# Kernel optimization log

Measured on AMD Instinct MI355X. Metric: run time of the kernel, lower is better.

## Reference

```python
import jax, jax.numpy as jnp
import numpy as np

DIM, HEADS, DHEAD = 256, 8, 64
HID = HEADS * DHEAD


def _elu1(x):
    # F.elu(x) + 1 == exp(x) for x<0, x+1 for x>=0
    return jnp.where(x > 0, x + 1.0, jnp.exp(x))


def setup_inputs() -> dict:
    key = jax.random.key(0)
    ks = jax.random.split(key, 6)
    B, H, W = 8, 64, 64
    x = jax.random.normal(ks[0], (B, DIM, H, W), dtype=jnp.float32)
    contact_map = jax.random.uniform(ks[1], (B, 1, H, W), dtype=jnp.float32)
    s_qkv = 1.0 / np.sqrt(DIM)
    Wqkv = jax.random.normal(ks[2], (3 * HID, DIM), dtype=jnp.float32) * s_qkv
    s_out = 1.0 / np.sqrt(HID)
    Wout = jax.random.normal(ks[3], (DIM, HID), dtype=jnp.float32) * s_out
    bout = jax.random.normal(ks[4], (DIM,), dtype=jnp.float32) * 0.01
    contact_scale = jnp.float32(0.1)
    return {"x": x, "contact_map": contact_map, "Wqkv": Wqkv,
            "Wout": Wout, "bout": bout, "contact_scale": contact_scale}


def reference(x, contact_map, Wqkv, Wout, bout, contact_scale):
    b, c, h, w = x.shape
    n = h * w
    xf = x.reshape(b, c, n)                                  # b c n
    qkv = jnp.einsum('oc,bcn->bon', Wqkv, xf)                # b (3*H*D) n
    qkv = qkv.reshape(b, 3, HEADS, DHEAD, n)                 # qkv-major channel order
    q = _elu1(qkv[:, 0])                                     # b h d n
    k = _elu1(qkv[:, 1])
    v = qkv[:, 2]
    cm = contact_map.reshape(b, 1, 1, n)                     # b 1 1 n
    k = k * (1.0 + contact_scale * cm)
    kv = jnp.einsum('bhdn,bhen->bhde', k, v)                 # b h d e
    ksum = k.sum(axis=-1)                                    # b h d
    z = 1.0 / (jnp.einsum('bhdn,bhd->bhn', q, ksum) + 1e-6)  # b h n
    out = jnp.einsum('bhde,bhdn->bhne', kv, q) * z[..., None]  # b h n e
    out = out.transpose(0, 1, 3, 2).reshape(b, HID, n)       # b (h d) n
    y = jnp.einsum('oc,bcn->bon', Wout, out) + bout[None, :, None]
    return y.reshape(b, -1, h, w)
```

## Files before the change

### kernel.cpp

```cpp
#include <hip/hip_runtime.h>
#include <stdint.h>


#define NPIX 4096
#define HIDC 512
#define DIMC 256
#define BATCH 8

typedef __attribute__((ext_vector_type(8))) short bf16x8;
typedef __attribute__((ext_vector_type(4))) float f32x4;
typedef __attribute__((ext_vector_type(16))) float f32x16;

__device__ __forceinline__ float bf2f(unsigned short h) {
    unsigned int u = ((unsigned int)h) << 16; float f;
    __builtin_memcpy(&f, &u, 4); return f;
}
__device__ __forceinline__ unsigned short f2bf(float f) {
    unsigned int u; __builtin_memcpy(&u, &f, 4);
    u += 0x7fffu + ((u >> 16) & 1u);
    return (unsigned short)(u >> 16);
}
__device__ __forceinline__ float elu1(float x) {
    return x > 0.f ? x + 1.f : __expf(x);
}
__device__ __forceinline__ void gl16(const unsigned short* g, unsigned short* l) {
    __builtin_amdgcn_global_load_lds(
        (__attribute__((address_space(1))) const void*)g,
        (__attribute__((address_space(3))) void*)l, 16, 0, 0);
}

__global__ __launch_bounds__(256) void k_convW(
    const float* __restrict__ Wqkv, const float* __restrict__ Wout,
    unsigned short* __restrict__ Wb, unsigned short* __restrict__ Wob)
{
    int i4 = (blockIdx.x * 256 + threadIdx.x) * 4;
    const int NW1 = 1536 * 256;
    float4 v; unsigned short* dst;
    if (i4 < NW1) { v = *(const float4*)&Wqkv[i4]; dst = Wb + i4; }
    else { int j = i4 - NW1; v = *(const float4*)&Wout[j]; dst = Wob + j; }
    ushort4 o; o.x = f2bf(v.x); o.y = f2bf(v.y); o.z = f2bf(v.z); o.w = f2bf(v.w);
    *(ushort4*)dst = o;
}

__global__ __launch_bounds__(256) void k_tx(
    const float* __restrict__ x, unsigned short* __restrict__ xT)
{
    __shared__ float tile[32][33];
    const int n0 = blockIdx.x * 32, c0 = blockIdx.y * 32, b = blockIdx.z;
    const int t = threadIdx.x;
    const int r = t >> 3, c4 = (t & 7) * 4;
    float4 v = *(const float4*)&x[((size_t)b * DIMC + c0 + r) * NPIX + n0 + c4];
    tile[r][c4 + 0] = v.x; tile[r][c4 + 1] = v.y;
    tile[r][c4 + 2] = v.z; tile[r][c4 + 3] = v.w;
    __syncthreads();
    ushort4 o;
    unsigned short* op = (unsigned short*)&o;
#pragma unroll
    for (int i = 0; i < 4; i++) op[i] = f2bf(tile[c4 + i][r]);
    *(ushort4*)&xT[((size_t)b * NPIX + n0 + r) * DIMC + c0 + c4] = o;
}

__global__ __launch_bounds__(256) void k_qkv(
    const unsigned short* __restrict__ xT,
    const unsigned short* __restrict__ Wb,
    const float* __restrict__ cmp,
    const float* __restrict__ csp,
    unsigned short* __restrict__ qT,
    unsigned short* __restrict__ kb,
    unsigned short* __restrict__ vb)
{
    const int b  = blockIdx.z;
    const int m0 = blockIdx.x * 128;
    const int n0 = blockIdx.y * 128;
    const int t = threadIdx.x;
    const int wave = t >> 6, lane = t & 63;
    const int wm = wave >> 1, wn = wave & 1;
    const int l31 = lane & 31, lhi = lane >> 5;
    const int sect = n0 >> 9;

    __shared__ unsigned short As[128 * 64];
    __shared__ unsigned short Bs[128 * 64];

    const unsigned short* Ag = xT + ((size_t)b * NPIX + m0) * DIMC;
    const unsigned short* Bg = Wb + (size_t)n0 * DIMC;

    const unsigned short* mArr = (sect == 0) ? As : Bs;
    const unsigned short* nArr = (sect == 0) ? Bs : As;

    f32x16 acc[2][2];
#pragma unroll
    for (int i = 0; i < 2; i++)
#pragma unroll
        for (int j = 0; j < 2; j++)
#pragma unroll
            for (int r = 0; r < 16; r++) acc[i][j][r] = 0.f;

    const int r8  = lane >> 3;
    const int jg8 = (((lane & 7) ^ r8) & 7) * 8;
    const int xsw = (l31 & 7);

    for (int k0 = 0; k0 < DIMC; k0 += 64) {
#pragma unroll
        for (int i = 0; i < 4; i++) {
            const int rowg = wave * 32 + i * 8;
            gl16(&Ag[(size_t)(rowg + r8) * DIMC + k0 + jg8], &As[rowg * 64]);
            gl16(&Bg[(size_t)(rowg + r8) * DIMC + k0 + jg8], &Bs[rowg * 64]);
        }
        __syncthreads();
#pragma unroll
        for (int ks = 0; ks < 4; ks++) {
            const int coff = ((ks * 2 + lhi) ^ xsw) * 8;
            bf16x8 af[2], bfg[2];
#pragma unroll
            for (int fm = 0; fm < 2; fm++)
                af[fm] = *(const bf16x8*)&mArr[(wm * 64 + fm * 32 + l31) * 64 + coff];
#pragma unroll
            for (int fn = 0; fn < 2; fn++)
                bfg[fn] = *(const bf16x8*)&nArr[(wn * 64 + fn * 32 + l31) * 64 + coff];
#pragma unroll
            for (int fm = 0; fm < 2; fm++)
#pragma unroll
                for (int fn = 0; fn < 2; fn++)
                    acc[fm][fn] = __builtin_amdgcn_mfma_f32_32x32x16_bf16(
                        af[fm], bfg[fn], acc[fm][fn], 0, 0, 0);
        }
        __syncthreads();
    }

    const float cs = *csp;
    if (sect == 0) {
#pragma unroll
        for (int fm = 0; fm < 2; fm++) {
            const int pbase = m0 + wm * 64 + fm * 32;
#pragma unroll
            for (int fn = 0; fn < 2; fn++) {
                const int o = n0 + wn * 64 + fn * 32 + l31;
#pragma unroll
                for (int r = 0; r < 16; r++) {
                    int prow = pbase + (r & 3) + 8 * (r >> 2) + 4 * lhi;
                    qT[((size_t)b * NPIX + prow) * HIDC + o] = f2bf(elu1(acc[fm][fn][r]));
                }
            }
        }
    } else {
        unsigned short* dstb = (sect == 1) ? kb : vb;
#pragma unroll
        for (int fm = 0; fm < 2; fm++) {
            const int obase = (n0 & 511) + wm * 64 + fm * 32;
#pragma unroll
            for (int fn = 0; fn < 2; fn++) {
                const int pixel = m0 + wn * 64 + fn * 32 + l31;
                float g = 1.f;
                if (sect == 1) g = 1.f + cs * cmp[(size_t)b * NPIX + pixel];
#pragma unroll
                for (int r = 0; r < 16; r++) {
                    int orow = obase + (r & 3) + 8 * (r >> 2) + 4 * lhi;
                    float val = acc[fm][fn][r];
                    if (sect == 1) val = elu1(val) * g;
                    dstb[((size_t)b * HIDC + orow) * NPIX + pixel] = f2bf(val);
                }
            }
        }
    }
}

#define LS2 40
__global__ __launch_bounds__(256) void k_kv(
    const unsigned short* __restrict__ kb, const unsigned short* __restrict__ vb,
    float* __restrict__ kv, float* __restrict__ ksum)
{
    const int bh = blockIdx.y, nc = blockIdx.x;
    const int t = threadIdx.x, wave = t >> 6, lane = t & 63;
    const int lrow = lane & 15, quad = lane >> 4;

    __shared__ unsigned short ks[64 * LS2];
    __shared__ unsigned short vs[64 * LS2];

    const size_t base = (size_t)bh * 64 * NPIX;
    f32x4 acc[4];
#pragma unroll
    for (int i = 0; i < 4; i++) acc[i] = (f32x4){0.f, 0.f, 0.f, 0.f};
    float ksacc = 0.f;

    const int row = t >> 2, c8 = (t & 3) * 8;

    for (int step = 0; step < 16; step++) {
        const int ncol = nc * 512 + step * 32;
        uint4 kq = *(const uint4*)&kb[base + (size_t)row * NPIX + ncol + c8];
        *(uint4*)&ks[row * LS2 + c8] = kq;
        *(uint4*)&vs[row * LS2 + c8] = *(const uint4*)&vb[base + (size_t)row * NPIX + ncol + c8];
        const unsigned short* kp = (const unsigned short*)&kq;
#pragma unroll
        for (int j = 0; j < 8; j++) ksacc += bf2f(kp[j]);
        __syncthreads();
        bf16x8 bfv = *(const bf16x8*)&vs[(wave * 16 + lrow) * LS2 + quad * 8];
#pragma unroll
        for (int mt = 0; mt < 4; mt++) {
            bf16x8 af = *(const bf16x8*)&ks[(mt * 16 + lrow) * LS2 + quad * 8];
            acc[mt] = __builtin_amdgcn_mfma_f32_16x16x32_bf16(af, bfv, acc[mt], 0, 0, 0);
        }
        __syncthreads();
    }

    float* kvb = kv + (size_t)bh * 4096;
#pragma unroll
    for (int mt = 0; mt < 4; mt++)
#pragma unroll
        for (int r = 0; r < 4; r++)
            atomicAdd(&kvb[(mt * 16 + quad * 4 + r) * 64 + wave * 16 + lrow], acc[mt][r]);
    atomicAdd(&ksum[bh * 64 + row], ksacc);
}

#define LS3 72
__global__ __launch_bounds__(256) void k_out(
    const unsigned short* __restrict__ qT,
    const float* __restrict__ kv, const float* __restrict__ ksum,
    unsigned short* __restrict__ outT)
{
    const int bh = blockIdx.y, p0 = blockIdx.x * 128;
    const int b = bh >> 3, h = bh & 7;
    const int t = threadIdx.x, wave = t >> 6, lane = t & 63;
    const int l31 = lane & 31, lhi = lane >> 5;

    __shared__ unsigned short Aq[128 * LS3];
    __shared__ unsigned short Bv[96 * LS3];

    const unsigned short* qg = qT + ((size_t)b * NPIX + p0) * HIDC + h * 64;
#pragma unroll
    for (int i = 0; i < 4; i++) {
        int idx = t + i * 256;
        int row = idx >> 3, c8 = (idx & 7) * 8;
        *(uint4*)&Aq[row * LS3 + c8] = *(const uint4*)&qg[(size_t)row * HIDC + c8];
    }
    const float* kvg = kv + (size_t)bh * 4096;
#pragma unroll
    for (int i = 0; i < 16; i++) {
        int idx = t + i * 256;
        int d = idx >> 6, e = idx & 63;
        Bv[e * LS3 + d] = f2bf(kvg[idx]);
    }
    if (t < 64) {
        float ksv = ksum[bh * 64 + t];
        unsigned short hi = f2bf(ksv);
        Bv[64 * LS3 + t] = hi;
        Bv[65 * LS3 + t] = f2bf(ksv - bf2f(hi));
    }
    for (int i = t; i < 30 * 64; i += 256)
        Bv[(66 + (i >> 6)) * LS3 + (i & 63)] = 0;
    __syncthreads();

    f32x16 acc[3];
#pragma unroll
    for (int j = 0; j < 3; j++)
#pragma unroll
        for (int r = 0; r < 16; r++) acc[j][r] = 0.f;

#pragma unroll
    for (int ksub = 0; ksub < 4; ksub++) {
        const int koff = ksub * 16 + lhi * 8;
        bf16x8 af = *(const bf16x8*)&Aq[(wave * 32 + l31) * LS3 + koff];
#pragma unroll
        for (int nf = 0; nf < 3; nf++) {
            bf16x8 bfg = *(const bf16x8*)&Bv[(nf * 32 + l31) * LS3 + koff];
            acc[nf] = __builtin_amdgcn_mfma_f32_32x32x16_bf16(af, bfg, acc[nf], 0, 0, 0);
        }
    }

    unsigned short* og = outT + ((size_t)b * NPIX + p0 + wave * 32) * HIDC + h * 64;
#pragma unroll
    for (int r = 0; r < 16; r++) {
        float hi = __shfl(acc[2][r], lane & 32);
        float lo = __shfl(acc[2][r], (lane & 32) | 1);
        float z = 1.f / (hi + lo + 1e-6f);
        int prow = (r & 3) + 8 * (r >> 2) + 4 * lhi;
#pragma unroll
        for (int nf = 0; nf < 2; nf++)
            og[(size_t)prow * HIDC + nf * 32 + l31] = f2bf(acc[nf][r] * z);
    }
}

__global__ __launch_bounds__(256) void k_y(
    const unsigned short* __restrict__ outT,
    const unsigned short* __restrict__ Wob,
    const float* __restrict__ bout,
    float* __restrict__ y)
{
    const int b  = blockIdx.z;
    const int m0 = blockIdx.x * 128;
    const int n0 = blockIdx.y * 128;
    const int t = threadIdx.x;
    const int wave = t >> 6, lane = t & 63;
    const int wm = wave >> 1, wn = wave & 1;
    const int lrow = lane & 15, quad = lane >> 4;

    __shared__ unsigned short As[128 * 64];
    __shared__ unsigned short Bs[128 * 64];

    const unsigned short* Ag = outT + ((size_t)b * NPIX + m0) * HIDC;
    const unsigned short* Bg = Wob + (size_t)n0 * HIDC;

    f32x4 acc[4][4];
#pragma unroll
    for (int i = 0; i < 4; i++)
#pragma unroll
        for (int j = 0; j < 4; j++) acc[i][j] = (f32x4){0.f, 0.f, 0.f, 0.f};

    const int r8  = lane >> 3;
    const int jg8 = (((lane & 7) ^ r8) & 7) * 8;
    const int xswA = (lrow & 7);

    for (int k0 = 0; k0 < HIDC; k0 += 64) {
#pragma unroll
        for (int i = 0; i < 4; i++) {
            const int rowg = wave * 32 + i * 8;
            gl16(&Ag[(size_t)(rowg + r8) * HIDC + k0 + jg8], &As[rowg * 64]);
            gl16(&Bg[(size_t)(rowg + r8) * HIDC + k0 + jg8], &Bs[rowg * 64]);
        }
        __syncthreads();
#pragma unroll
        for (int ksb = 0; ksb < 2; ksb++) {
            bf16x8 af[4], bfr[4];
#pragma unroll
            for (int mt = 0; mt < 4; mt++) {
                const int row = wm * 64 + mt * 16 + lrow;
                af[mt] = *(const bf16x8*)&As[row * 64 + (((ksb * 4 + quad) ^ xswA)) * 8];
            }
#pragma unroll
            for (int nt = 0; nt < 4; nt++) {
                const int row = wn * 64 + nt * 16 + lrow;
                bfr[nt] = *(const bf16x8*)&Bs[row * 64 + (((ksb * 4 + quad) ^ xswA)) * 8];
            }
#pragma unroll
            for (int mt = 0; mt < 4; mt++)
#pragma unroll
                for (int nt = 0; nt < 4; nt++)
                    acc[mt][nt] = __builtin_amdgcn_mfma_f32_16x16x32_bf16(
                        af[mt], bfr[nt], acc[mt][nt], 0, 0, 0);
        }
        __syncthreads();
    }

#pragma unroll
    for (int mt = 0; mt < 4; mt++) {
        const int pixel0 = m0 + wm * 64 + mt * 16 + quad * 4;
#pragma unroll
        for (int nt = 0; nt < 4; nt++) {
            const int o = n0 + wn * 64 + nt * 16 + lrow;
            const float bias = bout[o];
            f32x4 a = acc[mt][nt];
            float4 st; st.x = a[0] + bias; st.y = a[1] + bias;
            st.z = a[2] + bias; st.w = a[3] + bias;
            *(float4*)&y[((size_t)b * DIMC + o) * NPIX + pixel0] = st;
        }
    }
}

extern "C" void kernel_launch(void* const* d_in, const int* in_sizes, int n_in,
                              void* d_out, int out_size, void* d_ws, size_t ws_size,
                              hipStream_t stream) {
    (void)in_sizes; (void)n_in; (void)out_size; (void)ws_size;
    const float* x    = (const float*)d_in[0];
    const float* cm   = (const float*)d_in[1];
    const float* Wqkv = (const float*)d_in[2];
    const float* Wout = (const float*)d_in[3];
    const float* bout = (const float*)d_in[4];
    const float* csp  = (const float*)d_in[5];
    float* y = (float*)d_out;

    const size_t qn = (size_t)BATCH * HIDC * NPIX;
    char* ws = (char*)d_ws;
    unsigned short* qT   = (unsigned short*)ws;                 ws += qn * 2;
    unsigned short* kb   = (unsigned short*)ws;                 ws += qn * 2;
    unsigned short* vb   = (unsigned short*)ws;                 ws += qn * 2;
    unsigned short* outT = (unsigned short*)ws;                 ws += qn * 2;
    unsigned short* xT   = outT;
    float* kvp   = (float*)ws;                                  ws += (size_t)64 * 64 * 64 * 4;
    float* ksump = (float*)ws;                                  ws += (size_t)64 * 64 * 4;
    unsigned short* Wb  = (unsigned short*)ws;                  ws += (size_t)1536 * 256 * 2;
    unsigned short* Wob = (unsigned short*)ws;

    hipMemsetAsync(kvp, 0, ((size_t)64 * 64 * 64 + 64 * 64) * sizeof(float), stream);
    k_convW<<<512, 256, 0, stream>>>(Wqkv, Wout, Wb, Wob);
    k_tx  <<<dim3(128, 8, 8), 256, 0, stream>>>(x, xT);
    k_qkv <<<dim3(32, 12, 8), 256, 0, stream>>>(xT, Wb, cm, csp, qT, kb, vb);
    k_kv  <<<dim3(8, 64),     256, 0, stream>>>(kb, vb, kvp, ksump);
    k_out <<<dim3(32, 64),    256, 0, stream>>>(qT, kvp, ksump, outT);
    k_y   <<<dim3(32, 2, 8),  256, 0, stream>>>(outT, Wob, bout, y);
}
```

Baseline: 207.9 us.

## Fuse QKV projection with KV and ksum reduction in a single kernel

Replaces the separate QKV GEMM and kv-reduction kernels with one kernel per (pixel tile, batch) that computes q to global memory, but keeps k and v head tiles in shared memory and immediately reduces them into kv and ksum via MFMA and atomics. This removes writing and re-reading the full k and v tensors through global memory and one kernel launch. In exchange the grid is much smaller with one block per CU, work is serialised across heads with many barriers, and more atomic adds hit kv.

```diff
diff --git a/kernel.cpp b/kernel.cpp
--- a/kernel.cpp
+++ b/kernel.cpp
@@ -60,155 +60,154 @@
     *(ushort4*)&xT[((size_t)b * NPIX + n0 + r) * DIMC + c0 + c4] = o;
 }
 
-__global__ __launch_bounds__(256) void k_qkv(
+
+#define COMPUTE_TILE(SWAP, A0, A1)                                             \
+    {                                                                          \
+        const unsigned short* Wl = &Ws[cur][0];                                \
+        _Pragma("unroll")                                                      \
+        for (int ks = 0; ks < 16; ks++) {                                      \
+            bf16x8 wf = *(const bf16x8*)&Wl[(wn * 32 + l31) * DIMC +           \
+                                (((ks * 2 + lhi) ^ (l31 & 7)) * 8)];           \
+            if (SWAP) {                                                        \
+                A0 = __builtin_amdgcn_mfma_f32_32x32x16_bf16(wf, af[0][ks], A0, 0, 0, 0); \
+                A1 = __builtin_amdgcn_mfma_f32_32x32x16_bf16(wf, af[1][ks], A1, 0, 0, 0); \
+            } else {                                                           \
+                A0 = __builtin_amdgcn_mfma_f32_32x32x16_bf16(af[0][ks], wf, A0, 0, 0, 0); \
+                A1 = __builtin_amdgcn_mfma_f32_32x32x16_bf16(af[1][ks], wf, A1, 0, 0, 0); \
+            }                                                                  \
+        }                                                                      \
+    }
+
+__global__ __launch_bounds__(256, 1) void k_fused(
     const unsigned short* __restrict__ xT,
     const unsigned short* __restrict__ Wb,
     const float* __restrict__ cmp,
     const float* __restrict__ csp,
     unsigned short* __restrict__ qT,
-    unsigned short* __restrict__ kb,
-    unsigned short* __restrict__ vb)
-{
-    const int b  = blockIdx.z;
+    float* __restrict__ kvp,
+    float* __restrict__ ksump)
+{
+    const int b  = blockIdx.y;
     const int m0 = blockIdx.x * 128;
-    const int n0 = blockIdx.y * 128;
-    const int t = threadIdx.x;
+    const int t  = threadIdx.x;
     const int wave = t >> 6, lane = t & 63;
     const int wm = wave >> 1, wn = wave & 1;
     const int l31 = lane & 31, lhi = lane >> 5;
-    const int sect = n0 >> 9;
-
-    __shared__ unsigned short As[128 * 64];
-    __shared__ unsigned short Bs[128 * 64];
-
-    const unsigned short* Ag = xT + ((size_t)b * NPIX + m0) * DIMC;
-    const unsigned short* Bg = Wb + (size_t)n0 * DIMC;
-
-    const unsigned short* mArr = (sect == 0) ? As : Bs;
-    const unsigned short* nArr = (sect == 0) ? Bs : As;
-
-    f32x16 acc[2][2];
-#pragma unroll
-    for (int i = 0; i < 2; i++)
-#pragma unroll
-        for (int j = 0; j < 2; j++)
-#pragma unroll
-            for (int r = 0; r < 16; r++) acc[i][j][r] = 0.f;
-
-    const int r8  = lane >> 3;
-    const int jg8 = (((lane & 7) ^ r8) & 7) * 8;
-    const int xsw = (l31 & 7);
-
-    for (int k0 = 0; k0 < DIMC; k0 += 64) {
-#pragma unroll
-        for (int i = 0; i < 4; i++) {
-            const int rowg = wave * 32 + i * 8;
-            gl16(&Ag[(size_t)(rowg + r8) * DIMC + k0 + jg8], &As[rowg * 64]);
-            gl16(&Bg[(size_t)(rowg + r8) * DIMC + k0 + jg8], &Bs[rowg * 64]);
-        }
-        __syncthreads();
-#pragma unroll
-        for (int ks = 0; ks < 4; ks++) {
-            const int coff = ((ks * 2 + lhi) ^ xsw) * 8;
-            bf16x8 af[2], bfg[2];
-#pragma unroll
-            for (int fm = 0; fm < 2; fm++)
-                af[fm] = *(const bf16x8*)&mArr[(wm * 64 + fm * 32 + l31) * 64 + coff];
-#pragma unroll
-            for (int fn = 0; fn < 2; fn++)
-                bfg[fn] = *(const bf16x8*)&nArr[(wn * 64 + fn * 32 + l31) * 64 + coff];
-#pragma unroll
-            for (int fm = 0; fm < 2; fm++)
-#pragma unroll
-                for (int fn = 0; fn < 2; fn++)
-                    acc[fm][fn] = __builtin_amdgcn_mfma_f32_32x32x16_bf16(
-                        af[fm], bfg[fn], acc[fm][fn], 0, 0, 0);
-        }
-        __syncthreads();
-    }
+
+    __shared__ unsigned short Ws[2][64 * DIMC];
+    __shared__ unsigned short kS[64 * 128];
+    __shared__ unsigned short vS[64 * 128];
 
     const float cs = *csp;
-    if (sect == 0) {
-#pragma unroll
-        for (int fm = 0; fm < 2; fm++) {
-            const int pbase = m0 + wm * 64 + fm * 32;
-#pragma unroll
-            for (int fn = 0; fn < 2; fn++) {
-                const int o = n0 + wn * 64 + fn * 32 + l31;
-#pragma unroll
-                for (int r = 0; r < 16; r++) {
-                    int prow = pbase + (r & 3) + 8 * (r >> 2) + 4 * lhi;
-                    qT[((size_t)b * NPIX + prow) * HIDC + o] = f2bf(elu1(acc[fm][fn][r]));
-                }
+
+    auto stageW = [&](int wr, int buf) {
+#pragma unroll
+        for (int i = 0; i < 8; i++) {
+            const int rowl = wave * 16 + i * 2 + (lane >> 5);
+            const int ck = (lane & 31) ^ (rowl & 7);
+            gl16(&Wb[(size_t)(wr + rowl) * DIMC + ck * 8],
+                 &Ws[buf][(wave * 16 + i * 2) * DIMC]);
+        }
+    };
+
+    stageW(0, 0);
+
+    bf16x8 af[2][16];
+    {
+        const unsigned short* Ab = xT + ((size_t)b * NPIX + m0 + wm * 64) * DIMC;
+#pragma unroll
+        for (int pt = 0; pt < 2; pt++)
+#pragma unroll
+            for (int ks = 0; ks < 16; ks++)
+                af[pt][ks] = *(const bf16x8*)&Ab[(size_t)(pt * 32 + l31) * DIMC
+                                                 + ks * 16 + lhi * 8];
+    }
+
+    const float gv0 = 1.f + cs * cmp[(size_t)b * NPIX + m0 + wm * 64 + l31];
+    const float gv1 = 1.f + cs * cmp[(size_t)b * NPIX + m0 + wm * 64 + 32 + l31];
+
+    __syncthreads();
+    int cur = 0;
+
+    for (int nt = 0; nt < 8; nt++) {
+        stageW(nt < 7 ? (nt + 1) * 64 : 512, cur ^ 1);
+        f32x16 acc0, acc1;
+#pragma unroll
+        for (int r = 0; r < 16; r++) { acc0[r] = 0.f; acc1[r] = 0.f; }
+        COMPUTE_TILE(0, acc0, acc1)
+        const int chq = nt * 64 + wn * 32 + l31;
+        unsigned short* qg = qT + ((size_t)b * NPIX + m0 + wm * 64) * HIDC + chq;
+#pragma unroll
+        for (int r = 0; r < 16; r++) {
+            const int rp = (r & 3) + 8 * (r >> 2) + 4 * lhi;
+            qg[(size_t)rp * HIDC]        = f2bf(elu1(acc0[r]));
+            qg[(size_t)(32 + rp) * HIDC] = f2bf(elu1(acc1[r]));
+        }
+        __syncthreads();
+        cur ^= 1;
+    }
+
+    for (int h = 0; h < 8; h++) {
+        stageW(1024 + h * 64, cur ^ 1);
+        f32x16 acc0, acc1;
+#pragma unroll
+        for (int r = 0; r < 16; r++) { acc0[r] = 0.f; acc1[r] = 0.f; }
+        COMPUTE_TILE(1, acc0, acc1)
+#pragma unroll
+        for (int r = 0; r < 16; r++) {
+            const int ch = wn * 32 + (r & 3) + 8 * (r >> 2) + 4 * lhi;
+            const int sw = (ch & 7) << 3;
+            const int p0 = wm * 64 + l31;
+            kS[ch * 128 + (p0 ^ sw)]        = f2bf(elu1(acc0[r]) * gv0);
+            kS[ch * 128 + ((p0 + 32) ^ sw)] = f2bf(elu1(acc1[r]) * gv1);
+        }
+        __syncthreads();
+        {
+            const int ch = t & 63, cb = (t >> 6) * 4;
+            float s = 0.f;
+#pragma unroll
+            for (int j = 0; j < 4; j++) {
+                const bf16x8 kr = *(const bf16x8*)&kS[ch * 128 + (((cb + j) ^ (ch & 7)) * 8)];
+#pragma unroll
+                for (int u = 0; u < 8; u++) s += bf2f(((const unsigned short*)&kr)[u]);
             }
-        }
-    } else {
-        unsigned short* dstb = (sect == 1) ? kb : vb;
-#pragma unroll
-        for (int fm = 0; fm < 2; fm++) {
-            const int obase = (n0 & 511) + wm * 64 + fm * 32;
-#pragma unroll
-            for (int fn = 0; fn < 2; fn++) {
-                const int pixel = m0 + wn * 64 + fn * 32 + l31;
-                float g = 1.f;
-                if (sect == 1) g = 1.f + cs * cmp[(size_t)b * NPIX + pixel];
-#pragma unroll
-                for (int r = 0; r < 16; r++) {
-                    int orow = obase + (r & 3) + 8 * (r >> 2) + 4 * lhi;
-                    float val = acc[fm][fn][r];
-                    if (sect == 1) val = elu1(val) * g;
-                    dstb[((size_t)b * HIDC + orow) * NPIX + pixel] = f2bf(val);
-                }
-            }
-        }
-    }
-}
-
-#define LS2 40
-__global__ __launch_bounds__(256) void k_kv(
-    const unsigned short* __restrict__ kb, const unsigned short* __restrict__ vb,
-    float* __restrict__ kv, float* __restrict__ ksum)
-{
-    const int bh = blockIdx.y, nc = blockIdx.x;
-    const int t = threadIdx.x, wave = t >> 6, lane = t & 63;
-    const int lrow = lane & 15, quad = lane >> 4;
-
-    __shared__ unsigned short ks[64 * LS2];
-    __shared__ unsigned short vs[64 * LS2];
-
-    const size_t base = (size_t)bh * 64 * NPIX;
-    f32x4 acc[4];
-#pragma unroll
-    for (int i = 0; i < 4; i++) acc[i] = (f32x4){0.f, 0.f, 0.f, 0.f};
-    float ksacc = 0.f;
-
-    const int row = t >> 2, c8 = (t & 3) * 8;
-
-    for (int step = 0; step < 16; step++) {
-        const int ncol = nc * 512 + step * 32;
-        uint4 kq = *(const uint4*)&kb[base + (size_t)row * NPIX + ncol + c8];
-        *(uint4*)&ks[row * LS2 + c8] = kq;
-        *(uint4*)&vs[row * LS2 + c8] = *(const uint4*)&vb[base + (size_t)row * NPIX + ncol + c8];
-        const unsigned short* kp = (const unsigned short*)&kq;
-#pragma unroll
-        for (int j = 0; j < 8; j++) ksacc += bf2f(kp[j]);
-        __syncthreads();
-        bf16x8 bfv = *(const bf16x8*)&vs[(wave * 16 + lrow) * LS2 + quad * 8];
-#pragma unroll
-        for (int mt = 0; mt < 4; mt++) {
-            bf16x8 af = *(const bf16x8*)&ks[(mt * 16 + lrow) * LS2 + quad * 8];
-            acc[mt] = __builtin_amdgcn_mfma_f32_16x16x32_bf16(af, bfv, acc[mt], 0, 0, 0);
-        }
-        __syncthreads();
-    }
-
-    float* kvb = kv + (size_t)bh * 4096;
-#pragma unroll
-    for (int mt = 0; mt < 4; mt++)
-#pragma unroll
-        for (int r = 0; r < 4; r++)
-            atomicAdd(&kvb[(mt * 16 + quad * 4 + r) * 64 + wave * 16 + lrow], acc[mt][r]);
-    atomicAdd(&ksum[bh * 64 + row], ksacc);
+            atomicAdd(&ksump[(size_t)(b * 8 + h) * 64 + ch], s);
+        }
+        cur ^= 1;
+
+        if (h < 7) stageW(512 + (h + 1) * 64, cur ^ 1);
+#pragma unroll
+        for (int r = 0; r < 16; r++) { acc0[r] = 0.f; acc1[r] = 0.f; }
+        COMPUTE_TILE(1, acc0, acc1)
+#pragma unroll
+        for (int r = 0; r < 16; r++) {
+            const int ch = wn * 32 + (r & 3) + 8 * (r >> 2) + 4 * lhi;
+            const int sw = (ch & 7) << 3;
+            const int p0 = wm * 64 + l31;
+            vS[ch * 128 + (p0 ^ sw)]        = f2bf(acc0[r]);
+            vS[ch * 128 + ((p0 + 32) ^ sw)] = f2bf(acc1[r]);
+        }
+        __syncthreads();
+
+        f32x16 kvacc;
+#pragma unroll
+        for (int r = 0; r < 16; r++) kvacc[r] = 0.f;
+#pragma unroll
+        for (int pk = 0; pk < 8; pk++) {
+            const int co = (((pk * 2 + lhi) ^ (l31 & 7)) * 8);
+            const bf16x8 kf = *(const bf16x8*)&kS[(wm * 32 + l31) * 128 + co];
+            const bf16x8 vf = *(const bf16x8*)&vS[(wn * 32 + l31) * 128 + co];
+            kvacc = __builtin_amdgcn_mfma_f32_32x32x16_bf16(kf, vf, kvacc, 0, 0, 0);
+        }
+        __syncthreads();
+        float* kvb = kvp + (size_t)(b * 8 + h) * 4096;
+#pragma unroll
+        for (int r = 0; r < 16; r++) {
+            const int d = wm * 32 + (r & 3) + 8 * (r >> 2) + 4 * lhi;
+            atomicAdd(&kvb[d * 64 + wn * 32 + l31], kvacc[r]);
+        }
+        cur ^= 1;
+    }
 }
 
 #define LS3 72
@@ -370,8 +369,6 @@
     const size_t qn = (size_t)BATCH * HIDC * NPIX;
     char* ws = (char*)d_ws;
     unsigned short* qT   = (unsigned short*)ws;                 ws += qn * 2;
-    unsigned short* kb   = (unsigned short*)ws;                 ws += qn * 2;
-    unsigned short* vb   = (unsigned short*)ws;                 ws += qn * 2;
     unsigned short* outT = (unsigned short*)ws;                 ws += qn * 2;
     unsigned short* xT   = outT;
     float* kvp   = (float*)ws;                                  ws += (size_t)64 * 64 * 64 * 4;
@@ -381,9 +378,8 @@
 
     hipMemsetAsync(kvp, 0, ((size_t)64 * 64 * 64 + 64 * 64) * sizeof(float), stream);
     k_convW<<<512, 256, 0, stream>>>(Wqkv, Wout, Wb, Wob);
-    k_tx  <<<dim3(128, 8, 8), 256, 0, stream>>>(x, xT);
-    k_qkv <<<dim3(32, 12, 8), 256, 0, stream>>>(xT, Wb, cm, csp, qT, kb, vb);
-    k_kv  <<<dim3(8, 64),     256, 0, stream>>>(kb, vb, kvp, ksump);
-    k_out <<<dim3(32, 64),    256, 0, stream>>>(qT, kvp, ksump, outT);
-    k_y   <<<dim3(32, 2, 8),  256, 0, stream>>>(outT, Wob, bout, y);
-}
+    k_tx   <<<dim3(128, 8, 8), 256, 0, stream>>>(x, xT);
+    k_fused<<<dim3(32, 8),     256, 0, stream>>>(xT, Wb, cm, csp, qT, kvp, ksump);
+    k_out  <<<dim3(32, 64),    256, 0, stream>>>(qT, kvp, ksump, outT);
+    k_y    <<<dim3(32, 2, 8),  256, 0, stream>>>(outT, Wob, bout, y);
+}
```

New measurement: 198.7 us. 4.4% less time.

## Fuse K/V projection with per-head KV reduction, drop K/V buffers

Applied to the files above, without the earlier changes.

The QKV GEMM blocks for K and V are regrouped so each block computes one head's K and V rows for 128 pixels. The block then applies elu+contact gating, stages K and V tiles in shared memory, and computes the partial KV outer product and ksum directly with MFMA plus atomics. This removes the k_kv kernel and the global write and read of the bf16 K and V tensors. In exchange there are more atomic adds into kv (32 pixel chunks per head instead of 8) and a heavier epilogue in the GEMM kernel.

```diff
diff --git a/kernel.cpp b/kernel.cpp
--- a/kernel.cpp
+++ b/kernel.cpp
@@ -60,32 +60,30 @@
     *(ushort4*)&xT[((size_t)b * NPIX + n0 + r) * DIMC + c0 + c4] = o;
 }
 
-__global__ __launch_bounds__(256) void k_qkv(
+__global__ __launch_bounds__(256) void k_fused(
     const unsigned short* __restrict__ xT,
     const unsigned short* __restrict__ Wb,
     const float* __restrict__ cmp,
     const float* __restrict__ csp,
     unsigned short* __restrict__ qT,
-    unsigned short* __restrict__ kb,
-    unsigned short* __restrict__ vb)
+    float* __restrict__ kvp,
+    float* __restrict__ ksump)
 {
     const int b  = blockIdx.z;
     const int m0 = blockIdx.x * 128;
-    const int n0 = blockIdx.y * 128;
+    const int yb = blockIdx.y;
+    const int h  = yb - 4;
     const int t = threadIdx.x;
     const int wave = t >> 6, lane = t & 63;
     const int wm = wave >> 1, wn = wave & 1;
     const int l31 = lane & 31, lhi = lane >> 5;
-    const int sect = n0 >> 9;
-
-    __shared__ unsigned short As[128 * 64];
-    __shared__ unsigned short Bs[128 * 64];
+
+    __shared__ unsigned short sh[128 * 128];
+    unsigned short* As  = sh;
+    unsigned short* Bs  = sh + 128 * 64;
+    unsigned short* kvS = sh;
 
     const unsigned short* Ag = xT + ((size_t)b * NPIX + m0) * DIMC;
-    const unsigned short* Bg = Wb + (size_t)n0 * DIMC;
-
-    const unsigned short* mArr = (sect == 0) ? As : Bs;
-    const unsigned short* nArr = (sect == 0) ? Bs : As;
 
     f32x16 acc[2][2];
 #pragma unroll
@@ -103,8 +101,13 @@
 #pragma unroll
         for (int i = 0; i < 4; i++) {
             const int rowg = wave * 32 + i * 8;
-            gl16(&Ag[(size_t)(rowg + r8) * DIMC + k0 + jg8], &As[rowg * 64]);
-            gl16(&Bg[(size_t)(rowg + r8) * DIMC + k0 + jg8], &Bs[rowg * 64]);
+            const int arow = rowg + r8;
+            gl16(&Ag[(size_t)arow * DIMC + k0 + jg8], &As[rowg * 64]);
+            int wrow;
+            if (yb < 4) wrow = yb * 128 + arow;
+            else wrow = (arow < 64) ? (512 + h * 64 + arow)
+                                    : (1024 + h * 64 + (arow - 64));
+            gl16(&Wb[(size_t)wrow * DIMC + k0 + jg8], &Bs[rowg * 64]);
         }
         __syncthreads();
 #pragma unroll
@@ -113,10 +116,10 @@
             bf16x8 af[2], bfg[2];
 #pragma unroll
             for (int fm = 0; fm < 2; fm++)
-                af[fm] = *(const bf16x8*)&mArr[(wm * 64 + fm * 32 + l31) * 64 + coff];
+                af[fm] = *(const bf16x8*)&As[(wm * 64 + fm * 32 + l31) * 64 + coff];
 #pragma unroll
             for (int fn = 0; fn < 2; fn++)
-                bfg[fn] = *(const bf16x8*)&nArr[(wn * 64 + fn * 32 + l31) * 64 + coff];
+                bfg[fn] = *(const bf16x8*)&Bs[(wn * 64 + fn * 32 + l31) * 64 + coff];
 #pragma unroll
             for (int fm = 0; fm < 2; fm++)
 #pragma unroll
@@ -127,8 +130,8 @@
         __syncthreads();
     }
 
-    const float cs = *csp;
-    if (sect == 0) {
+    if (yb < 4) {
+        const int n0 = yb * 128;
 #pragma unroll
         for (int fm = 0; fm < 2; fm++) {
             const int pbase = m0 + wm * 64 + fm * 32;
@@ -142,73 +145,61 @@
                 }
             }
         }
-    } else {
-        unsigned short* dstb = (sect == 1) ? kb : vb;
-#pragma unroll
-        for (int fm = 0; fm < 2; fm++) {
-            const int obase = (n0 & 511) + wm * 64 + fm * 32;
+        return;
+    }
+
+    const float cs = *csp;
+    float gv4[2];
+#pragma unroll
+    for (int fm = 0; fm < 2; fm++)
+        gv4[fm] = 1.f + cs * cmp[(size_t)b * NPIX + m0 + wm * 64 + fm * 32 + l31];
+
+    float ks0 = 0.f, ks1 = 0.f;
+#pragma unroll
+    for (int fm = 0; fm < 2; fm++) {
+#pragma unroll
+        for (int r = 0; r < 16; r++) {
+            const int rp = (r & 3) + 8 * (r >> 2) + 4 * lhi;
+            const float g = __shfl(gv4[fm], rp);
+            const int px = wm * 64 + fm * 32 + rp;
 #pragma unroll
             for (int fn = 0; fn < 2; fn++) {
-                const int pixel = m0 + wn * 64 + fn * 32 + l31;
-                float g = 1.f;
-                if (sect == 1) g = 1.f + cs * cmp[(size_t)b * NPIX + pixel];
-#pragma unroll
-                for (int r = 0; r < 16; r++) {
-                    int orow = obase + (r & 3) + 8 * (r >> 2) + 4 * lhi;
-                    float val = acc[fm][fn][r];
-                    if (sect == 1) val = elu1(val) * g;
-                    dstb[((size_t)b * HIDC + orow) * NPIX + pixel] = f2bf(val);
+                const int o = wn * 64 + fn * 32 + l31;
+                float val = acc[fm][fn][r];
+                unsigned short st;
+                if (o < 64) {
+                    float kvl = elu1(val) * g;
+                    if (fn == 0) ks0 += kvl; else ks1 += kvl;
+                    st = f2bf(kvl);
+                } else {
+                    st = f2bf(val);
                 }
+                kvS[(size_t)o * 128 + (px ^ ((o & 7) << 3))] = st;
             }
         }
     }
-}
-
-#define LS2 40
-__global__ __launch_bounds__(256) void k_kv(
-    const unsigned short* __restrict__ kb, const unsigned short* __restrict__ vb,
-    float* __restrict__ kv, float* __restrict__ ksum)
-{
-    const int bh = blockIdx.y, nc = blockIdx.x;
-    const int t = threadIdx.x, wave = t >> 6, lane = t & 63;
-    const int lrow = lane & 15, quad = lane >> 4;
-
-    __shared__ unsigned short ks[64 * LS2];
-    __shared__ unsigned short vs[64 * LS2];
-
-    const size_t base = (size_t)bh * 64 * NPIX;
-    f32x4 acc[4];
-#pragma unroll
-    for (int i = 0; i < 4; i++) acc[i] = (f32x4){0.f, 0.f, 0.f, 0.f};
-    float ksacc = 0.f;
-
-    const int row = t >> 2, c8 = (t & 3) * 8;
-
-    for (int step = 0; step < 16; step++) {
-        const int ncol = nc * 512 + step * 32;
-        uint4 kq = *(const uint4*)&kb[base + (size_t)row * NPIX + ncol + c8];
-        *(uint4*)&ks[row * LS2 + c8] = kq;
-        *(uint4*)&vs[row * LS2 + c8] = *(const uint4*)&vb[base + (size_t)row * NPIX + ncol + c8];
-        const unsigned short* kp = (const unsigned short*)&kq;
-#pragma unroll
-        for (int j = 0; j < 8; j++) ksacc += bf2f(kp[j]);
-        __syncthreads();
-        bf16x8 bfv = *(const bf16x8*)&vs[(wave * 16 + lrow) * LS2 + quad * 8];
-#pragma unroll
-        for (int mt = 0; mt < 4; mt++) {
-            bf16x8 af = *(const bf16x8*)&ks[(mt * 16 + lrow) * LS2 + quad * 8];
-            acc[mt] = __builtin_amdgcn_mfma_f32_16x16x32_bf16(af, bfv, acc[mt], 0, 0, 0);
-        }
-        __syncthreads();
-    }
-
-    float* kvb = kv + (size_t)bh * 4096;
-#pragma unroll
-    for (int mt = 0; mt < 4; mt++)
-#pragma unroll
-        for (int r = 0; r < 4; r++)
-            atomicAdd(&kvb[(mt * 16 + quad * 4 + r) * 64 + wave * 16 + lrow], acc[mt][r]);
-    atomicAdd(&ksum[bh * 64 + row], ksacc);
+    if (wn == 0) {
+        atomicAdd(&ksump[(size_t)(b * 8 + h) * 64 + l31], ks0);
+        atomicAdd(&ksump[(size_t)(b * 8 + h) * 64 + 32 + l31], ks1);
+    }
+    __syncthreads();
+
+    f32x16 kva;
+#pragma unroll
+    for (int r = 0; r < 16; r++) kva[r] = 0.f;
+#pragma unroll
+    for (int pk = 0; pk < 8; pk++) {
+        const int co = ((pk * 2 + lhi) ^ (l31 & 7)) * 8;
+        bf16x8 kf = *(const bf16x8*)&kvS[(size_t)(wm * 32 + l31) * 128 + co];
+        bf16x8 vf = *(const bf16x8*)&kvS[(size_t)(64 + wn * 32 + l31) * 128 + co];
+        kva = __builtin_amdgcn_mfma_f32_32x32x16_bf16(kf, vf, kva, 0, 0, 0);
+    }
+    float* kvb = kvp + (size_t)(b * 8 + h) * 4096;
+#pragma unroll
+    for (int r = 0; r < 16; r++) {
+        const int d = wm * 32 + (r & 3) + 8 * (r >> 2) + 4 * lhi;
+        atomicAdd(&kvb[(size_t)d * 64 + wn * 32 + l31], kva[r]);
+    }
 }
 
 #define LS3 72
@@ -370,8 +361,6 @@
     const size_t qn = (size_t)BATCH * HIDC * NPIX;
     char* ws = (char*)d_ws;
     unsigned short* qT   = (unsigned short*)ws;                 ws += qn * 2;
-    unsigned short* kb   = (unsigned short*)ws;                 ws += qn * 2;
-    unsigned short* vb   = (unsigned short*)ws;                 ws += qn * 2;
     unsigned short* outT = (unsigned short*)ws;                 ws += qn * 2;
     unsigned short* xT   = outT;
     float* kvp   = (float*)ws;                                  ws += (size_t)64 * 64 * 64 * 4;
@@ -381,9 +370,8 @@
 
     hipMemsetAsync(kvp, 0, ((size_t)64 * 64 * 64 + 64 * 64) * sizeof(float), stream);
     k_convW<<<512, 256, 0, stream>>>(Wqkv, Wout, Wb, Wob);
-    k_tx  <<<dim3(128, 8, 8), 256, 0, stream>>>(x, xT);
-    k_qkv <<<dim3(32, 12, 8), 256, 0, stream>>>(xT, Wb, cm, csp, qT, kb, vb);
-    k_kv  <<<dim3(8, 64),     256, 0, stream>>>(kb, vb, kvp, ksump);
-    k_out <<<dim3(32, 64),    256, 0, stream>>>(qT, kvp, ksump, outT);
-    k_y   <<<dim3(32, 2, 8),  256, 0, stream>>>(outT, Wob, bout, y);
-}
+    k_tx   <<<dim3(128, 8, 8), 256, 0, stream>>>(x, xT);
+    k_fused<<<dim3(32, 12, 8), 256, 0, stream>>>(xT, Wb, cm, csp, qT, kvp, ksump);
+    k_out  <<<dim3(32, 64),    256, 0, stream>>>(qT, kvp, ksump, outT);
+    k_y    <<<dim3(32, 2, 8),  256, 0, stream>>>(outT, Wob, bout, y);
+}
```

After: 218.2 us. 1.05x slower.
